# Kernel tuning notes

Hardware: AMD Instinct MI355X
Metric: run time of the kernel (lower is better)

The kernel has to match this reference:

```python
import jax, jax.numpy as jnp
import numpy as np

EXPERT_NUM = 8
TOPK = 2
N_EMBD = 768
D_FF = 3072
B, S = 2, 1024
T = B * S


def setup_inputs() -> dict:
    key = jax.random.key(0)
    ks = jax.random.split(key, 6)
    x = jax.random.normal(ks[0], (B, S, N_EMBD), dtype=jnp.float32)
    # gumbel noise, matching gumbel_noise(n, k) in the torch module
    u = jax.random.uniform(ks[1], (T, EXPERT_NUM), dtype=jnp.float32,
                           minval=1e-6, maxval=1.0 - 1e-6)
    noise = -jnp.log(-jnp.log(u))
    router_w = jax.random.normal(ks[2], (EXPERT_NUM, N_EMBD), dtype=jnp.float32) * (N_EMBD ** -0.5)
    w1 = jax.random.normal(ks[3], (EXPERT_NUM, N_EMBD, D_FF), dtype=jnp.float32) * (N_EMBD ** -0.5)
    b1 = jnp.zeros((EXPERT_NUM, D_FF), dtype=jnp.float32)
    w2 = jax.random.normal(ks[4], (EXPERT_NUM, D_FF, N_EMBD), dtype=jnp.float32) * (D_FF ** -0.5)
    b2 = jnp.zeros((EXPERT_NUM, N_EMBD), dtype=jnp.float32)
    return {"x": x, "noise": noise, "router_w": router_w,
            "w1": w1, "b1": b1, "w2": w2, "b2": b2}


def reference(x, noise, router_w, w1, b1, w2, b2):
    d = x.shape[-1]
    xs = x.reshape(-1, d)                                   # [T, d]
    gate_logits = xs @ router_w.T + noise                   # [T, E]
    # topk_exp > 1 branch: topk first, then softmax over the k kept logits
    weights, selected = jax.lax.top_k(gate_logits, TOPK)    # [T, k]
    weights = jax.nn.softmax(weights.astype(jnp.float32), axis=1).astype(x.dtype)
    out = jnp.zeros_like(xs)
    for e in range(EXPERT_NUM):
        # combine weight of expert e per token (0 where not selected)
        w_e = jnp.sum(jnp.where(selected == e, weights, 0.0), axis=1)  # [T]
        h = jax.nn.gelu(xs @ w1[e] + b1[e])                 # [T, d_ff]
        y = h @ w2[e] + b2[e]                               # [T, d]
        out = out + w_e[:, None] * y
    return out.reshape(x.shape)
```

## Files before the change

### kernel.cpp

```cpp
#include <hip/hip_runtime.h>
#include <hip/hip_bf16.h>

#define T_TOK 2048
#define NE 768
#define DFF 3072
#define NEXP 8
#define ROWS_PAD 4480
#define MAX_TILES 24

typedef __attribute__((ext_vector_type(8))) __bf16 bf16x8;
typedef __attribute__((ext_vector_type(4))) __bf16 bf16x4;
typedef __attribute__((ext_vector_type(4))) float f32x4;

__device__ __forceinline__ float gelu_tanh(float v) {
  float u = 0.7978845608028654f * (v + 0.044715f * v * v * v);
  float e = __expf(-2.0f * fabsf(u));
  float t = (1.0f - e) / (1.0f + e);
  t = copysignf(t, u);
  return 0.5f * v * (1.0f + t);
}

__global__ void router_kernel(const float* __restrict__ x,
                              const float* __restrict__ noise,
                              const float* __restrict__ rw,
                              int* __restrict__ sel, float* __restrict__ wgt) {
  int tok  = (blockIdx.x * blockDim.x + threadIdx.x) >> 6;
  int lane = threadIdx.x & 63;
  const float* xr = x + (size_t)tok * NE;
  float acc[NEXP];
#pragma unroll
  for (int e = 0; e < NEXP; e++) acc[e] = 0.f;
  for (int d = lane; d < NE; d += 64) {
    float xv = xr[d];
#pragma unroll
    for (int e = 0; e < NEXP; e++) acc[e] += xv * rw[e * NE + d];
  }
#pragma unroll
  for (int e = 0; e < NEXP; e++) {
#pragma unroll
    for (int off = 32; off > 0; off >>= 1) acc[e] += __shfl_xor(acc[e], off);
  }
  if (lane == 0) {
    float lg[NEXP];
#pragma unroll
    for (int e = 0; e < NEXP; e++) lg[e] = acc[e] + noise[tok * NEXP + e];
    int i0 = 0;
#pragma unroll
    for (int e = 1; e < NEXP; e++) if (lg[e] > lg[i0]) i0 = e;
    int i1 = (i0 == 0) ? 1 : 0;
#pragma unroll
    for (int e = 0; e < NEXP; e++) if (e != i0 && lg[e] > lg[i1]) i1 = e;
    float ex = __expf(lg[i1] - lg[i0]);
    float w0 = 1.f / (1.f + ex);
    sel[tok * 2]     = i0; sel[tok * 2 + 1] = i1;
    wgt[tok * 2]     = w0; wgt[tok * 2 + 1] = 1.f - w0;
  }
}

__global__ void assign_kernel(const int* __restrict__ sel,
                              int* __restrict__ offs, int* __restrict__ pair_tok,
                              int* __restrict__ slot_of, int* __restrict__ tiles,
                              int* __restrict__ ntl) {
  __shared__ int scnt[NEXP];
  __shared__ int soff[NEXP + 1];
  int e = threadIdx.x >> 6;
  int lane = threadIdx.x & 63;

  int count = 0;
  for (int t0 = 0; t0 < T_TOK; t0 += 64) {
    int t = t0 + lane;
    bool m = (sel[t * 2] == e) | (sel[t * 2 + 1] == e);
    count += __popcll(__ballot(m));
  }
  if (lane == 0) scnt[e] = count;
  __syncthreads();

  if (threadIdx.x == 0) {
    int s = 0;
    for (int k = 0; k < NEXP; k++) { soff[k] = s; s += scnt[k]; }
    soff[NEXP] = s;
    for (int i = 0; i <= NEXP; i++) offs[i] = soff[i];
    int k2 = 0;
    for (int k = 0; k < NEXP; k++)
      for (int r = soff[k]; r < soff[k + 1]; r += 256) {
        tiles[k2 * 2] = k; tiles[k2 * 2 + 1] = r; k2++;
      }
    *ntl = k2;
  }
  __syncthreads();

  int base = soff[e];
  for (int t0 = 0; t0 < T_TOK; t0 += 64) {
    int t = t0 + lane;
    int s0 = sel[t * 2], s1 = sel[t * 2 + 1];
    bool m0 = (s0 == e), m1 = (s1 == e);
    bool m = m0 | m1;
    unsigned long long mask = __ballot(m);
    int pos = __popcll(mask & ((1ull << lane) - 1ull));
    if (m) {
      int slot = base + pos;
      pair_tok[slot] = t;
      slot_of[t * 2 + (m0 ? 0 : 1)] = slot;
    }
    base += __popcll(mask);
  }
}

__global__ void gather_kernel(const float* __restrict__ x, const int* __restrict__ pair_tok,
                              __hip_bfloat16* __restrict__ xg) {
  int r = blockIdx.x;
  int tok = pair_tok[r];
  const float4* s = (const float4*)(x + (size_t)tok * NE);
  __hip_bfloat16* d = xg + (size_t)r * NE;
  int t = threadIdx.x;
  if (t < NE / 4) {
    float4 v = s[t];
    bf16x4 o;
    o[0] = (__bf16)__float2bfloat16(v.x); o[1] = (__bf16)__float2bfloat16(v.y);
    o[2] = (__bf16)__float2bfloat16(v.z); o[3] = (__bf16)__float2bfloat16(v.w);
    *reinterpret_cast<bf16x4*>(&d[t * 4]) = o;
  }
}

__global__ void transpose_cvt(const float* __restrict__ src, __hip_bfloat16* __restrict__ dst,
                              int K, int N) {
  __shared__ __hip_bfloat16 tile[64 * 72];
  int ntk = K >> 6, ntn = N >> 6;
  int bid = blockIdx.x;
  int e = bid / (ntk * ntn);
  int rem = bid % (ntk * ntn);
  int tk = rem / ntn, tn = rem % ntn;
  const float* s = src + (size_t)e * K * N + (size_t)(tk * 64) * N + tn * 64;
  int t = threadIdx.x;
  int a = t & 15;
  int kp = t >> 4;
#pragma unroll
  for (int i = 0; i < 2; i++) {
    int k = 2 * kp + 32 * i;
    float4 v0 = *reinterpret_cast<const float4*>(&s[(size_t)k * N + 4 * a]);
    float4 v1 = *reinterpret_cast<const float4*>(&s[(size_t)(k + 1) * N + 4 * a]);
    const float* p0 = &v0.x; const float* p1 = &v1.x;
#pragma unroll
    for (int j = 0; j < 4; j++) {
      __hip_bfloat162 p;
      p.x = __float2bfloat16(p0[j]); p.y = __float2bfloat16(p1[j]);
      *reinterpret_cast<__hip_bfloat162*>(&tile[(4 * a + j) * 72 + k]) = p;
    }
  }
  __syncthreads();
  int n = t >> 3, g = t & 7;
  __hip_bfloat16* d = dst + (size_t)e * N * K + (size_t)(tn * 64) * K + tk * 64;
#pragma unroll
  for (int i = 0; i < 2; i++) {
    int row = n + 32 * i;
    bf16x8 v = *reinterpret_cast<const bf16x8*>(&tile[row * 72 + g * 8]);
    *reinterpret_cast<bf16x8*>(&d[(size_t)row * K + g * 8]) = v;
  }
}

template <int K, int N, int MODE, int SPLITS>
__global__ __launch_bounds__(512, 1) void ffn_gemm(
    const __hip_bfloat16* __restrict__ A, const __hip_bfloat16* __restrict__ Bt,
    const float* __restrict__ bias, __hip_bfloat16* __restrict__ DST,
    const int* __restrict__ offs, const int* __restrict__ tiles,
    const int* __restrict__ ntl) {
  constexpr int NT = N / 256;
  constexpr int KS = K / SPLITS;
  constexpr int NS = KS / 64;
  int bid = blockIdx.x;
  int nt = bid % NT;
  int r1 = bid / NT;
  int sp = r1 % SPLITS;
  int ti = r1 / SPLITS;
  if (ti >= *ntl) return;
  int e = tiles[ti * 2], row0 = tiles[ti * 2 + 1];
  int rend = offs[e + 1];
  int n0 = nt * 256;
  int kbeg = sp * KS;

  __shared__ __align__(16) __hip_bfloat16 lds[2][2][256 * 64];

  int tid = threadIdx.x;
  int w = tid >> 6, l = tid & 63;
  int wr = w >> 2, wc = w & 3;
  int r16 = l & 15, q = l >> 4;
  int swz = r16 & 7;

  f32x4 acc[8][4];
#pragma unroll
  for (int m = 0; m < 8; m++)
#pragma unroll
    for (int n = 0; n < 4; n++) acc[m][n] = (f32x4){0.f, 0.f, 0.f, 0.f};

  const __hip_bfloat16* Bte = Bt + (size_t)e * N * K;

  auto STAGE = [&](int b, int k0) {
    char* cA = (char*)lds[b][0];
    char* cB = (char*)lds[b][1];
#pragma unroll
    for (int i = 0; i < 4; i++) {
      int c = tid + 512 * i;
      int row = c >> 3, p = c & 7;
      const __hip_bfloat16* ga =
          A + (size_t)(row0 + row) * K + k0 + ((p ^ (row & 7)) << 3);
      __builtin_amdgcn_global_load_lds(
          (const __attribute__((address_space(1))) void*)ga,
          (__attribute__((address_space(3))) void*)(cA + c * 16), 16, 0, 0);
    }
#pragma unroll
    for (int i = 0; i < 4; i++) {
      int c = tid + 512 * i;
      int row = c >> 3, p = c & 7;
      const __hip_bfloat16* gb =
          Bte + (size_t)(n0 + row) * K + k0 + ((p ^ (row & 7)) << 3);
      __builtin_amdgcn_global_load_lds(
          (const __attribute__((address_space(1))) void*)gb,
          (__attribute__((address_space(3))) void*)(cB + c * 16), 16, 0, 0);
    }
  };

  STAGE(0, kbeg);
  for (int t = 0; t < NS; t++) {
    if (t + 1 < NS) {
      STAGE((t + 1) & 1, kbeg + (t + 1) * 64);
      asm volatile("s_waitcnt vmcnt(8)" ::: "memory");
    } else {
      asm volatile("s_waitcnt vmcnt(0)" ::: "memory");
    }
    __builtin_amdgcn_s_barrier();
    __builtin_amdgcn_sched_barrier(0);
    const char* cA = (const char*)lds[t & 1][0];
    const char* cB = (const char*)lds[t & 1][1];
#pragma unroll
    for (int kk = 0; kk < 2; kk++) {
      int inner = ((kk * 4 + q) ^ swz) << 4;
      bf16x8 aF[8], bF[4];
#pragma unroll
      for (int m = 0; m < 8; m++)
        aF[m] = *reinterpret_cast<const bf16x8*>(cA + (wr * 128 + m * 16 + r16) * 128 + inner);
#pragma unroll
      for (int n = 0; n < 4; n++)
        bF[n] = *reinterpret_cast<const bf16x8*>(cB + (wc * 64 + n * 16 + r16) * 128 + inner);
#pragma unroll
      for (int m = 0; m < 8; m++)
#pragma unroll
        for (int n = 0; n < 4; n++)
          acc[m][n] = __builtin_amdgcn_mfma_f32_16x16x32_bf16(aF[m], bF[n], acc[m][n], 0, 0, 0);
    }
    __builtin_amdgcn_s_barrier();
  }

  float* ldsF = (float*)&lds[0][0][0];
  __hip_bfloat16* dst = DST + (size_t)sp * ROWS_PAD * N;
#pragma unroll
  for (int hh = 0; hh < 4; hh++) {
    __syncthreads();
    if (wr == (hh >> 1)) {
      int mbase = (hh & 1) * 4;
#pragma unroll
      for (int mi = 0; mi < 4; mi++)
#pragma unroll
        for (int n = 0; n < 4; n++)
#pragma unroll
          for (int rg = 0; rg < 4; rg++)
            ldsF[(mi * 16 + q * 4 + rg) * 264 + wc * 64 + n * 16 + r16] =
                acc[mbase + mi][n][rg];
    }
    __syncthreads();
#pragma unroll
    for (int i = 0; i < 4; i++) {
      int s = tid + 512 * i;
      int r = s >> 5, c8 = s & 31;
      int rr = row0 + hh * 64 + r;
      if (rr < rend) {
        const float* src = &ldsF[r * 264 + c8 * 8];
        float4 v0 = *reinterpret_cast<const float4*>(src);
        float4 v1 = *reinterpret_cast<const float4*>(src + 4);
        const float* bp = &bias[e * N + n0 + c8 * 8];
        float4 bb0 = *reinterpret_cast<const float4*>(bp);
        float4 bb1 = *reinterpret_cast<const float4*>(bp + 4);
        float vv[8]  = {v0.x, v0.y, v0.z, v0.w, v1.x, v1.y, v1.z, v1.w};
        float bbv[8] = {bb0.x, bb0.y, bb0.z, bb0.w, bb1.x, bb1.y, bb1.z, bb1.w};
        bf16x8 o;
#pragma unroll
        for (int j = 0; j < 8; j++) {
          float val;
          if (MODE == 0) val = gelu_tanh(vv[j] + bbv[j]);
          else           val = vv[j] + (sp == 0 ? bbv[j] : 0.f);
          o[j] = (__bf16)__float2bfloat16(val);
        }
        *reinterpret_cast<bf16x8*>(&dst[(size_t)rr * N + n0 + c8 * 8]) = o;
      }
    }
  }
}

template <int SPLITS>
__global__ void combine_kernel(const __hip_bfloat16* __restrict__ yb,
                               const int* __restrict__ slot_of,
                               const float* __restrict__ wgt,
                               float* __restrict__ out) {
  int t = blockIdx.x;
  int d = threadIdx.x;
  int s0 = slot_of[2 * t], s1 = slot_of[2 * t + 1];
  float w0 = wgt[2 * t], w1 = wgt[2 * t + 1];
  float a0 = 0.f, a1 = 0.f, a2 = 0.f, a3 = 0.f;
#pragma unroll
  for (int sp = 0; sp < SPLITS; sp++) {
    bf16x4 p = reinterpret_cast<const bf16x4*>(yb + (size_t)(sp * ROWS_PAD + s0) * NE)[d];
    bf16x4 r = reinterpret_cast<const bf16x4*>(yb + (size_t)(sp * ROWS_PAD + s1) * NE)[d];
    a0 += w0 * (float)p[0] + w1 * (float)r[0];
    a1 += w0 * (float)p[1] + w1 * (float)r[1];
    a2 += w0 * (float)p[2] + w1 * (float)r[2];
    a3 += w0 * (float)p[3] + w1 * (float)r[3];
  }
  float4 o = {a0, a1, a2, a3};
  reinterpret_cast<float4*>(out)[(size_t)t * (NE / 4) + d] = o;
}

extern "C" void kernel_launch(void* const* d_in, const int* in_sizes, int n_in,
                              void* d_out, int out_size, void* d_ws, size_t ws_size,
                              hipStream_t stream) {
  const float* x     = (const float*)d_in[0];
  const float* noise = (const float*)d_in[1];
  const float* rw    = (const float*)d_in[2];
  const float* w1    = (const float*)d_in[3];
  const float* b1    = (const float*)d_in[4];
  const float* w2    = (const float*)d_in[5];
  const float* b2    = (const float*)d_in[6];
  float* out = (float*)d_out;

  constexpr int SP2 = 4;

  char* ws = (char*)d_ws;
  size_t off = 0;
  auto carve = [&](size_t bytes) { void* p = ws + off; off = (off + bytes + 255) & ~255ull; return p; };
  int*   offs     = (int*)carve((NEXP + 1) * 4);
  int*   sel      = (int*)carve(T_TOK * 2 * 4);
  float* wgt      = (float*)carve(T_TOK * 2 * 4);
  int*   pair_tok = (int*)carve(ROWS_PAD * 4);
  int*   slot_of  = (int*)carve(T_TOK * 2 * 4);
  int*   tiles    = (int*)carve(MAX_TILES * 2 * 4);
  int*   ntl      = (int*)carve(4);
  __hip_bfloat16* xg  = (__hip_bfloat16*)carve((size_t)ROWS_PAD * NE * 2);
  __hip_bfloat16* h   = (__hip_bfloat16*)carve((size_t)ROWS_PAD * DFF * 2);
  __hip_bfloat16* yb  = (__hip_bfloat16*)carve((size_t)SP2 * ROWS_PAD * NE * 2);
  __hip_bfloat16* wt  = (__hip_bfloat16*)carve((size_t)NEXP * NE * DFF * 2);

  if (off > ws_size) {
    hipMemsetAsync(d_out, 0, (size_t)out_size * sizeof(float), stream);
    return;
  }

  router_kernel<<<(T_TOK * 64) / 256, 256, 0, stream>>>(x, noise, rw, sel, wgt);
  assign_kernel<<<1, 512, 0, stream>>>(sel, offs, pair_tok, slot_of, tiles, ntl);
  gather_kernel<<<T_TOK * 2, 256, 0, stream>>>(x, pair_tok, xg);

  transpose_cvt<<<NEXP * (NE / 64) * (DFF / 64), 256, 0, stream>>>(w1, wt, NE, DFF);
  ffn_gemm<NE, DFF, 0, 1><<<MAX_TILES * 1 * (DFF / 256), 512, 0, stream>>>(
      xg, wt, b1, h, offs, tiles, ntl);

  transpose_cvt<<<NEXP * (DFF / 64) * (NE / 64), 256, 0, stream>>>(w2, wt, DFF, NE);
  ffn_gemm<DFF, NE, 1, SP2><<<MAX_TILES * SP2 * (NE / 256), 512, 0, stream>>>(
      h, wt, b2, yb, offs, tiles, ntl);

  combine_kernel<SP2><<<T_TOK, 192, 0, stream>>>(yb, slot_of, wgt, out);
}
```

Baseline: 152.0 us.

## Restructure expert GEMM into 8-phase interleaved load/MFMA pipeline with XCD-aware block remap

The grouped FFN GEMM now splits each 64-wide K step into two 32-wide halves and four compute phases. Each phase issues a slice of the next tile's global-to-LDS loads between fragment reads and prioritized MFMA bursts, with barriers and partial vmcnt waits in between. Block indices are remapped round-robin across the 8 XCDs so that blocks sharing a weight tile land on the same chiplet's L2. The LDS swizzle is rewritten for the new 32-column layout. The aim is to hide memory latency behind MFMA work and improve L2 reuse, at the price of many more barriers per iteration and a fragile hand-written wait schedule.

```diff
diff --git a/kernel.cpp b/kernel.cpp
--- a/kernel.cpp
+++ b/kernel.cpp
@@ -18,6 +18,10 @@
   float t = (1.0f - e) / (1.0f + e);
   t = copysignf(t, u);
   return 0.5f * v * (1.0f + t);
+}
+
+__device__ __forceinline__ int swz_chunk(int c) {
+  return (c & ~7) | ((c & 7) ^ ((c >> 3) & 7));
 }
 
 __global__ void router_kernel(const float* __restrict__ x,
@@ -159,7 +163,7 @@
 }
 
 template <int K, int N, int MODE, int SPLITS>
-__global__ __launch_bounds__(512, 1) void ffn_gemm(
+__global__ __launch_bounds__(512, 1) void ffn_gemm8(
     const __hip_bfloat16* __restrict__ A, const __hip_bfloat16* __restrict__ Bt,
     const float* __restrict__ bias, __hip_bfloat16* __restrict__ DST,
     const int* __restrict__ offs, const int* __restrict__ tiles,
@@ -167,24 +171,28 @@
   constexpr int NT = N / 256;
   constexpr int KS = K / SPLITS;
   constexpr int NS = KS / 64;
-  int bid = blockIdx.x;
-  int nt = bid % NT;
-  int r1 = bid / NT;
+  constexpr int NWG = MAX_TILES * SPLITS * NT;
+
+  int b = blockIdx.x;
+  int l = (b & 7) * (NWG >> 3) + (b >> 3);
+  int ti = l % MAX_TILES;
+  int r1 = l / MAX_TILES;
   int sp = r1 % SPLITS;
-  int ti = r1 / SPLITS;
+  int nt = r1 / SPLITS;
   if (ti >= *ntl) return;
   int e = tiles[ti * 2], row0 = tiles[ti * 2 + 1];
   int rend = offs[e + 1];
   int n0 = nt * 256;
   int kbeg = sp * KS;
 
-  __shared__ __align__(16) __hip_bfloat16 lds[2][2][256 * 64];
+  __shared__ __align__(16) char smem[131072];
+  char* smA = smem;
+  char* smB = smem + 65536;
 
   int tid = threadIdx.x;
-  int w = tid >> 6, l = tid & 63;
+  int w = tid >> 6, l64 = tid & 63;
   int wr = w >> 2, wc = w & 3;
-  int r16 = l & 15, q = l >> 4;
-  int swz = r16 & 7;
+  int r16 = l64 & 15, q = l64 >> 4;
 
   f32x4 acc[8][4];
 #pragma unroll
@@ -194,63 +202,108 @@
 
   const __hip_bfloat16* Bte = Bt + (size_t)e * N * K;
 
-  auto STAGE = [&](int b, int k0) {
-    char* cA = (char*)lds[b][0];
-    char* cB = (char*)lds[b][1];
-#pragma unroll
-    for (int i = 0; i < 4; i++) {
-      int c = tid + 512 * i;
-      int row = c >> 3, p = c & 7;
-      const __hip_bfloat16* ga =
-          A + (size_t)(row0 + row) * K + k0 + ((p ^ (row & 7)) << 3);
+  auto ISSUE = [&](int op, int buf, int kh, int tt) {
+    char* dst0 = (op == 0 ? smA : smB) + (buf * 2 + kh) * 16384;
+    const __hip_bfloat16* g =
+        (op == 0) ? (A + (size_t)row0 * K) : (Bte + (size_t)n0 * K);
+    int kbase = kbeg + tt * 64 + kh * 32;
+#pragma unroll
+    for (int i = 0; i < 2; i++) {
+      int Lc = tid + 512 * i;
+      int fc = swz_chunk(Lc);
+      int row = fc >> 2, p = fc & 3;
+      const __hip_bfloat16* src = g + (size_t)row * K + kbase + p * 8;
       __builtin_amdgcn_global_load_lds(
-          (const __attribute__((address_space(1))) void*)ga,
-          (__attribute__((address_space(3))) void*)(cA + c * 16), 16, 0, 0);
-    }
-#pragma unroll
-    for (int i = 0; i < 4; i++) {
-      int c = tid + 512 * i;
-      int row = c >> 3, p = c & 7;
-      const __hip_bfloat16* gb =
-          Bte + (size_t)(n0 + row) * K + k0 + ((p ^ (row & 7)) << 3);
-      __builtin_amdgcn_global_load_lds(
-          (const __attribute__((address_space(1))) void*)gb,
-          (__attribute__((address_space(3))) void*)(cB + c * 16), 16, 0, 0);
+          (const __attribute__((address_space(1))) void*)src,
+          (__attribute__((address_space(3))) void*)(dst0 + Lc * 16), 16, 0, 0);
     }
   };
 
-  STAGE(0, kbeg);
+  ISSUE(0, 0, 0, 0); ISSUE(1, 0, 0, 0); ISSUE(0, 0, 1, 0); ISSUE(1, 0, 1, 0);
+  asm volatile("s_waitcnt vmcnt(4)" ::: "memory");
+  __builtin_amdgcn_s_barrier();
+
   for (int t = 0; t < NS; t++) {
-    if (t + 1 < NS) {
-      STAGE((t + 1) & 1, kbeg + (t + 1) * 64);
-      asm volatile("s_waitcnt vmcnt(8)" ::: "memory");
-    } else {
-      asm volatile("s_waitcnt vmcnt(0)" ::: "memory");
-    }
-    __builtin_amdgcn_s_barrier();
-    __builtin_amdgcn_sched_barrier(0);
-    const char* cA = (const char*)lds[t & 1][0];
-    const char* cB = (const char*)lds[t & 1][1];
-#pragma unroll
-    for (int kk = 0; kk < 2; kk++) {
-      int inner = ((kk * 4 + q) ^ swz) << 4;
-      bf16x8 aF[8], bF[4];
-#pragma unroll
-      for (int m = 0; m < 8; m++)
-        aF[m] = *reinterpret_cast<const bf16x8*>(cA + (wr * 128 + m * 16 + r16) * 128 + inner);
+    const bool more = (t + 1 < NS);
+    const char* rdA = smA + (t & 1) * 32768;
+    const char* rdB = smB + (t & 1) * 32768;
+    const int wb = (t + 1) & 1;
+    bf16x8 aF[4], bF[4];
+
+#pragma unroll
+    for (int m = 0; m < 4; m++)
+      aF[m] = *reinterpret_cast<const bf16x8*>(
+          rdA + swz_chunk((wr * 128 + m * 16 + r16) * 4 + q) * 16);
+#pragma unroll
+    for (int n = 0; n < 4; n++)
+      bF[n] = *reinterpret_cast<const bf16x8*>(
+          rdB + swz_chunk((wc * 64 + n * 16 + r16) * 4 + q) * 16);
+    if (more) ISSUE(0, wb, 0, t + 1);
+    __builtin_amdgcn_s_barrier();
+    __builtin_amdgcn_s_setprio(1);
+#pragma unroll
+    for (int m = 0; m < 4; m++)
 #pragma unroll
       for (int n = 0; n < 4; n++)
-        bF[n] = *reinterpret_cast<const bf16x8*>(cB + (wc * 64 + n * 16 + r16) * 128 + inner);
-#pragma unroll
-      for (int m = 0; m < 8; m++)
-#pragma unroll
-        for (int n = 0; n < 4; n++)
-          acc[m][n] = __builtin_amdgcn_mfma_f32_16x16x32_bf16(aF[m], bF[n], acc[m][n], 0, 0, 0);
-    }
-    __builtin_amdgcn_s_barrier();
-  }
-
-  float* ldsF = (float*)&lds[0][0][0];
+        acc[m][n] = __builtin_amdgcn_mfma_f32_16x16x32_bf16(aF[m], bF[n], acc[m][n], 0, 0, 0);
+    __builtin_amdgcn_s_setprio(0);
+    __builtin_amdgcn_s_barrier();
+
+#pragma unroll
+    for (int m = 0; m < 4; m++)
+      aF[m] = *reinterpret_cast<const bf16x8*>(
+          rdA + swz_chunk((wr * 128 + (4 + m) * 16 + r16) * 4 + q) * 16);
+    if (more) ISSUE(1, wb, 0, t + 1);
+    __builtin_amdgcn_s_barrier();
+    __builtin_amdgcn_s_setprio(1);
+#pragma unroll
+    for (int m = 0; m < 4; m++)
+#pragma unroll
+      for (int n = 0; n < 4; n++)
+        acc[4 + m][n] = __builtin_amdgcn_mfma_f32_16x16x32_bf16(aF[m], bF[n], acc[4 + m][n], 0, 0, 0);
+    __builtin_amdgcn_s_setprio(0);
+    if (more) asm volatile("s_waitcnt vmcnt(4)" ::: "memory");
+    else      asm volatile("s_waitcnt vmcnt(0)" ::: "memory");
+    __builtin_amdgcn_s_barrier();
+
+#pragma unroll
+    for (int m = 0; m < 4; m++)
+      aF[m] = *reinterpret_cast<const bf16x8*>(
+          rdA + 16384 + swz_chunk((wr * 128 + m * 16 + r16) * 4 + q) * 16);
+#pragma unroll
+    for (int n = 0; n < 4; n++)
+      bF[n] = *reinterpret_cast<const bf16x8*>(
+          rdB + 16384 + swz_chunk((wc * 64 + n * 16 + r16) * 4 + q) * 16);
+    if (more) ISSUE(0, wb, 1, t + 1);
+    __builtin_amdgcn_s_barrier();
+    __builtin_amdgcn_s_setprio(1);
+#pragma unroll
+    for (int m = 0; m < 4; m++)
+#pragma unroll
+      for (int n = 0; n < 4; n++)
+        acc[m][n] = __builtin_amdgcn_mfma_f32_16x16x32_bf16(aF[m], bF[n], acc[m][n], 0, 0, 0);
+    __builtin_amdgcn_s_setprio(0);
+    __builtin_amdgcn_s_barrier();
+
+#pragma unroll
+    for (int m = 0; m < 4; m++)
+      aF[m] = *reinterpret_cast<const bf16x8*>(
+          rdA + 16384 + swz_chunk((wr * 128 + (4 + m) * 16 + r16) * 4 + q) * 16);
+    if (more) ISSUE(1, wb, 1, t + 1);
+    __builtin_amdgcn_s_barrier();
+    __builtin_amdgcn_s_setprio(1);
+#pragma unroll
+    for (int m = 0; m < 4; m++)
+#pragma unroll
+      for (int n = 0; n < 4; n++)
+        acc[4 + m][n] = __builtin_amdgcn_mfma_f32_16x16x32_bf16(aF[m], bF[n], acc[4 + m][n], 0, 0, 0);
+    __builtin_amdgcn_s_setprio(0);
+    if (more) asm volatile("s_waitcnt vmcnt(4)" ::: "memory");
+    else      asm volatile("s_waitcnt vmcnt(0)" ::: "memory");
+    __builtin_amdgcn_s_barrier();
+  }
+
+  float* ldsF = (float*)smem;
   __hip_bfloat16* dst = DST + (size_t)sp * ROWS_PAD * N;
 #pragma unroll
   for (int hh = 0; hh < 4; hh++) {
@@ -357,11 +410,11 @@
   gather_kernel<<<T_TOK * 2, 256, 0, stream>>>(x, pair_tok, xg);
 
   transpose_cvt<<<NEXP * (NE / 64) * (DFF / 64), 256, 0, stream>>>(w1, wt, NE, DFF);
-  ffn_gemm<NE, DFF, 0, 1><<<MAX_TILES * 1 * (DFF / 256), 512, 0, stream>>>(
+  ffn_gemm8<NE, DFF, 0, 1><<<MAX_TILES * 1 * (DFF / 256), 512, 0, stream>>>(
       xg, wt, b1, h, offs, tiles, ntl);
 
   transpose_cvt<<<NEXP * (DFF / 64) * (NE / 64), 256, 0, stream>>>(w2, wt, DFF, NE);
-  ffn_gemm<DFF, NE, 1, SP2><<<MAX_TILES * SP2 * (NE / 256), 512, 0, stream>>>(
+  ffn_gemm8<DFF, NE, 1, SP2><<<MAX_TILES * SP2 * (NE / 256), 512, 0, stream>>>(
       h, wt, b2, yb, offs, tiles, ntl);
 
   combine_kernel<SP2><<<T_TOK, 192, 0, stream>>>(yb, slot_of, wgt, out);
```

Measured after the change: 145.6 us. -4.2%, faster.
